# Kernel tuning notes

Measured on AMD Instinct MI355X. Metric: run time of the kernel, lower is better.

Reference implementation:

```python
import jax, jax.numpy as jnp
import numpy as np


def setup_inputs() -> dict:
    key = jax.random.key(0)
    k0, k1, k2, k3 = jax.random.split(key, 4)
    B, T, M, E, H = 4, 2048, 1024, 8, 4096
    x = jax.random.normal(k0, (B, T, M), dtype=jnp.float32)
    wg = jax.random.normal(k1, (M, E), dtype=jnp.float32) * 0.02
    w1 = jax.random.normal(k2, (E, M, H), dtype=jnp.float32) * 0.02
    w2 = jax.random.normal(k3, (E, H, M), dtype=jnp.float32) * 0.02
    return {"x": x, "wg": wg, "w1": w1, "w2": w2}


def reference(x, wg, w1, w2):
    """GShard MoE layer: top-1 gate + dense one-hot dispatch/combine + expert FFN."""
    M = x.shape[-1]
    xs = x.reshape(-1, M)                      # [s, m]
    s = xs.shape[0]
    E = wg.shape[1]
    capacity = s // E                          # capacity_factor = 1.0

    # ---- top-1 gate (deepspeed/gshard top1gating) ----
    logits = xs @ wg                           # [s, e]
    gates = jax.nn.softmax(logits, axis=-1)
    idx = jnp.argmax(gates, axis=1)            # [s]
    mask1 = jax.nn.one_hot(idx, E, dtype=gates.dtype)  # [s, e]
    me = gates.mean(axis=0)
    ce = mask1.mean(axis=0)
    l_aux = jnp.sum(me * ce) * E
    # position of each token within its expert's buffer
    locations = jnp.cumsum(mask1, axis=0) - 1.0          # [s, e]
    mask1 = mask1 * (locations < capacity).astype(gates.dtype)  # drop overflow
    gates1 = gates * mask1                                 # [s, e]
    loc_s = jnp.sum(locations * mask1, axis=1).astype(jnp.int32)  # [s]
    loc_sc = jax.nn.one_hot(loc_s, capacity, dtype=gates.dtype)   # [s, c]
    combine = gates1[:, :, None] * loc_sc[:, None, :]       # [s, e, c]
    dispatch = (combine > 0).astype(x.dtype)                # [s, e, c]

    # ---- dense one-hot dispatch (the kernel-headroom hotspot) ----
    dispatched = jnp.einsum('sec,sm->ecm', dispatch, xs)    # [e, c, m]

    # ---- per-expert 2-layer FFN ----
    h = jax.nn.relu(jnp.einsum('ecm,emh->ech', dispatched, w1))
    expert_out = jnp.einsum('ech,ehm->ecm', h, w2)          # [e, c, m]

    # ---- dense one-hot combine ----
    out = jnp.einsum('sec,ecm->sm', combine, expert_out).reshape(x.shape)
    return out, l_aux
```

## Files before the change

kernel.cpp:

```cpp
#include <hip/hip_runtime.h>
#include <hip/hip_bf16.h>

#define S_TOK 8192
#define MDIM  1024
#define EXP   8
#define HDIM  4096
#define CAP   1024

typedef __attribute__((ext_vector_type(8))) short short8;
typedef __attribute__((ext_vector_type(4))) float floatx4;

#define BARRIER() asm volatile("s_barrier" ::: "memory")
#define WAITV6()  asm volatile("s_waitcnt vmcnt(6)" ::: "memory")
#define WAITV0()  asm volatile("s_waitcnt vmcnt(0)" ::: "memory")
#define SCHEDB()  __builtin_amdgcn_sched_barrier(0)

__device__ __forceinline__ unsigned short f2b(float f) {
    union { float f; unsigned int i; } v; v.f = f;
    unsigned int r = v.i + 0x7fffu + ((v.i >> 16) & 1u);
    return (unsigned short)(r >> 16);
}

__device__ __forceinline__ void gl2lds16(const unsigned short* g, unsigned short* l) {
    __builtin_amdgcn_global_load_lds(
        (const __attribute__((address_space(1))) unsigned int*)g,
        (__attribute__((address_space(3))) unsigned int*)l,
        16, 0, 0);
}

__global__ __launch_bounds__(256) void gate_kernel(
    const float* __restrict__ x, const float* __restrict__ wg,
    float* __restrict__ gates8, int* __restrict__ token_expert)
{
    const int wave = threadIdx.x >> 6, lane = threadIdx.x & 63;
    const int s = blockIdx.x * 4 + wave;

    const float* xr = x + (size_t)s * MDIM + lane * 16;
    float xv[16];
#pragma unroll
    for (int q = 0; q < 4; ++q) *(float4*)(xv + q * 4) = *(const float4*)(xr + q * 4);

    float acc[EXP];
#pragma unroll
    for (int e = 0; e < EXP; ++e) acc[e] = 0.f;
    const int m0 = lane * 16;
#pragma unroll
    for (int j = 0; j < 16; ++j) {
        const float xm = xv[j];
        const float* wr = wg + (size_t)(m0 + j) * EXP;
        float4 w0 = *(const float4*)(wr);
        float4 w1v = *(const float4*)(wr + 4);
        acc[0] += xm * w0.x; acc[1] += xm * w0.y; acc[2] += xm * w0.z; acc[3] += xm * w0.w;
        acc[4] += xm * w1v.x; acc[5] += xm * w1v.y; acc[6] += xm * w1v.z; acc[7] += xm * w1v.w;
    }
#pragma unroll
    for (int e = 0; e < EXP; ++e) {
#pragma unroll
        for (int off = 32; off > 0; off >>= 1)
            acc[e] += __shfl_down(acc[e], off);
    }
    if (lane == 0) {
        float mx = acc[0]; int idx = 0;
#pragma unroll
        for (int e = 1; e < EXP; ++e) if (acc[e] > mx) { mx = acc[e]; idx = e; }
        float g[EXP]; float sum = 0.f;
#pragma unroll
        for (int e = 0; e < EXP; ++e) { g[e] = expf(acc[e] - mx); sum += g[e]; }
        float inv = 1.f / sum;
#pragma unroll
        for (int e = 0; e < EXP; ++e) gates8[(size_t)s * EXP + e] = g[e] * inv;
        token_expert[s] = idx;
    }
}

__global__ __launch_bounds__(256) void scan_kernel(
    const float* __restrict__ gates8, const int* __restrict__ token_expert,
    int* __restrict__ slot_token, float* __restrict__ slot_gate,
    float* __restrict__ laux_out)
{
    __shared__ int   cnt[256][EXP];
    __shared__ float fsum[256][EXP];
    __shared__ int   tot[EXP];
    const int t = threadIdx.x;

    for (int i = t; i < EXP * CAP; i += 256) slot_token[i] = -1;

    int local[EXP];
#pragma unroll
    for (int e = 0; e < EXP; ++e) local[e] = 0;
    const int s0 = t * 32;
    for (int j = 0; j < 32; ++j) local[token_expert[s0 + j]]++;
#pragma unroll
    for (int e = 0; e < EXP; ++e) cnt[t][e] = local[e];
    __syncthreads();

    if (t < EXP) {
        int run = 0;
        for (int i = 0; i < 256; ++i) { int v = cnt[i][t]; cnt[i][t] = run; run += v; }
        tot[t] = run;
    }
    __syncthreads();

    int off[EXP];
#pragma unroll
    for (int e = 0; e < EXP; ++e) off[e] = cnt[t][e];
    for (int j = 0; j < 32; ++j) {
        int s = s0 + j;
        int e = token_expert[s];
        int loc = off[e]++;
        if (loc < CAP) {
            int slot = e * CAP + loc;
            slot_token[slot] = s;
            slot_gate[slot]  = gates8[(size_t)s * EXP + e];
        }
    }

    float ms[EXP];
#pragma unroll
    for (int e = 0; e < EXP; ++e) ms[e] = 0.f;
    for (int j = 0; j < 32; ++j) {
        const float* g = gates8 + (size_t)(s0 + j) * EXP;
#pragma unroll
        for (int e = 0; e < EXP; ++e) ms[e] += g[e];
    }
#pragma unroll
    for (int e = 0; e < EXP; ++e) fsum[t][e] = ms[e];
    __syncthreads();
    for (int st = 128; st > 0; st >>= 1) {
        if (t < st) {
#pragma unroll
            for (int e = 0; e < EXP; ++e) fsum[t][e] += fsum[t + st][e];
        }
        __syncthreads();
    }
    if (t == 0) {
        float l = 0.f;
#pragma unroll
        for (int e = 0; e < EXP; ++e)
            l += (fsum[0][e] / (float)S_TOK) * ((float)tot[e] / (float)S_TOK);
        laux_out[0] = l * (float)EXP;
    }
}

__global__ __launch_bounds__(256) void dispatch_cvt(
    const float* __restrict__ x, const int* __restrict__ slot_token,
    unsigned short* __restrict__ xd)
{
    const int slot = blockIdx.x, t = threadIdx.x;
    const int tok = slot_token[slot];
    unsigned short v[4];
    if (tok >= 0) {
        float4 f = *(const float4*)(x + (size_t)tok * MDIM + t * 4);
        v[0] = f2b(f.x); v[1] = f2b(f.y); v[2] = f2b(f.z); v[3] = f2b(f.w);
    } else {
        v[0] = v[1] = v[2] = v[3] = 0;
    }
    *(int2*)(xd + (size_t)slot * MDIM + t * 4) = *(const int2*)v;
}

__global__ __launch_bounds__(256) void transpose_cvt(
    const float* __restrict__ src, unsigned short* __restrict__ dst, int R, int C)
{
    __shared__ unsigned short Ls[64 * 72];
    const size_t eo = (size_t)blockIdx.z * R * C;
    src += eo; dst += eo;
    const int C0 = blockIdx.x * 64, R0 = blockIdx.y * 64;
    const int t = threadIdx.x;
    {
        const int r = t >> 2, c0 = (t & 3) * 16;
        const float* p = src + (size_t)(R0 + r) * C + C0 + c0;
        float f[16];
#pragma unroll
        for (int q = 0; q < 4; ++q) *(float4*)(f + q * 4) = ((const float4*)p)[q];
#pragma unroll
        for (int j = 0; j < 16; ++j) Ls[(c0 + j) * 72 + r] = f2b(f[j]);
    }
    __syncthreads();
    {
        const int c = t >> 2, m0 = (t & 3) * 16;
        int4 v0 = *(const int4*)&Ls[c * 72 + m0];
        int4 v1 = *(const int4*)&Ls[c * 72 + m0 + 8];
        int4* q = (int4*)(dst + (size_t)(C0 + c) * R + R0 + m0);
        q[0] = v0; q[1] = v1;
    }
}

template<int KT, int N, bool SCATTER>
__global__ __launch_bounds__(512, 2) void ffn_gemm_8p(
    const unsigned short* __restrict__ Ag, const unsigned short* __restrict__ BT,
    void* __restrict__ Outv,
    const int* __restrict__ slot_token, const float* __restrict__ slot_gate)
{
    constexpr int K   = KT * 64;
    constexpr int NBX = N / 128;
    constexpr int NWG = NBX * (CAP / 256);

    extern __shared__ __align__(16) unsigned short sm[];
    unsigned short* Abuf = sm;
    unsigned short* Bbuf = sm + 3 * 16384;

    const int e    = blockIdx.z;
    const int orig = blockIdx.x;
    const int logical = (orig & 7) * (NWG >> 3) + (orig >> 3);
    const int nb = (logical % NBX) * 128;
    const int ib = (logical / NBX) * 256;

    const int tid  = threadIdx.x;
    const int lane = tid & 63, wave = tid >> 6;
    const int quad = lane >> 4, l15 = lane & 15;
    const int wm = wave >> 2, wn = wave & 3;

    const int rr   = tid >> 3;
    const int slot = (tid & 7) ^ (rr & 7);
    const unsigned short* Asrc = Ag + (size_t)(e * CAP + ib + rr) * K + slot * 8;
    const unsigned short* Bsrc = BT + ((size_t)e * N + nb + rr) * K + slot * 8;

    auto stageA = [&](int buf, int t, int ca) {
        gl2lds16(Asrc + (size_t)ca * 64 * K + t * 64,
                 Abuf + buf * 16384 + ca * 4096 + wave * 512);
    };
    auto stageB = [&](int buf, int t, int cb) {
        gl2lds16(Bsrc + (size_t)cb * 64 * K + t * 64,
                 Bbuf + buf * 8192 + cb * 4096 + wave * 512);
    };

    const int sx  = l15 & 7;
    const int ko0 = ((0 + quad) ^ sx) * 8;
    const int ko1 = ((4 + quad) ^ sx) * 8;
    const int arow = wm * 128 + l15;
    const int brow = wn * 32 + l15;

    floatx4 acc[8][2];
#pragma unroll
    for (int i = 0; i < 8; ++i)
#pragma unroll
        for (int j = 0; j < 2; ++j)
            acc[i][j] = (floatx4){0.f, 0.f, 0.f, 0.f};

#pragma unroll
    for (int ca = 0; ca < 4; ++ca) stageA(0, 0, ca);
#pragma unroll
    for (int cb = 0; cb < 2; ++cb) stageB(0, 0, cb);
#pragma unroll
    for (int ca = 0; ca < 4; ++ca) stageA(1, 1, ca);
#pragma unroll
    for (int cb = 0; cb < 2; ++cb) stageB(1, 1, cb);
    WAITV6();
    BARRIER();

    int buf = 0;
    for (int t = 0; t < KT; ++t) {
        const int nbuf = (buf >= 1) ? buf - 1 : 2;
        const bool st  = (t + 2 < KT);

        short8 brg[2][2];
#pragma unroll
        for (int fn = 0; fn < 2; ++fn) {
            const int row = brow + fn * 16;
            brg[fn][0] = *(const short8*)&Bbuf[buf * 8192 + row * 64 + ko0];
            brg[fn][1] = *(const short8*)&Bbuf[buf * 8192 + row * 64 + ko1];
        }
        short8 aA[8];
#pragma unroll
        for (int fm = 0; fm < 4; ++fm) {
            const int row = arow + fm * 16;
            aA[fm * 2 + 0] = *(const short8*)&Abuf[buf * 16384 + row * 64 + ko0];
            aA[fm * 2 + 1] = *(const short8*)&Abuf[buf * 16384 + row * 64 + ko1];
        }
        if (st) { stageA(nbuf, t + 2, 0); stageA(nbuf, t + 2, 1); }
        BARRIER(); SCHEDB();
        __builtin_amdgcn_s_setprio(1);
#pragma unroll
        for (int fm = 0; fm < 4; ++fm) {
            acc[fm][0] = __builtin_amdgcn_mfma_f32_16x16x32_bf16(aA[fm*2+0], brg[0][0], acc[fm][0], 0, 0, 0);
            acc[fm][0] = __builtin_amdgcn_mfma_f32_16x16x32_bf16(aA[fm*2+1], brg[0][1], acc[fm][0], 0, 0, 0);
        }
        __builtin_amdgcn_s_setprio(0); SCHEDB(); BARRIER();

        short8 aB[8];
#pragma unroll
        for (int fm = 0; fm < 4; ++fm) {
            const int row = arow + 64 + fm * 16;
            aB[fm * 2 + 0] = *(const short8*)&Abuf[buf * 16384 + row * 64 + ko0];
            aB[fm * 2 + 1] = *(const short8*)&Abuf[buf * 16384 + row * 64 + ko1];
        }
        if (st) { stageA(nbuf, t + 2, 2); stageA(nbuf, t + 2, 3); }
        BARRIER(); SCHEDB();
        __builtin_amdgcn_s_setprio(1);
#pragma unroll
        for (int fm = 0; fm < 4; ++fm) {
            acc[fm][1] = __builtin_amdgcn_mfma_f32_16x16x32_bf16(aA[fm*2+0], brg[1][0], acc[fm][1], 0, 0, 0);
            acc[fm][1] = __builtin_amdgcn_mfma_f32_16x16x32_bf16(aA[fm*2+1], brg[1][1], acc[fm][1], 0, 0, 0);
        }
        __builtin_amdgcn_s_setprio(0); SCHEDB(); BARRIER();

        if (st) stageB(nbuf, t + 2, 0);
        BARRIER(); SCHEDB();
        __builtin_amdgcn_s_setprio(1);
#pragma unroll
        for (int fm = 0; fm < 4; ++fm) {
            acc[4+fm][0] = __builtin_amdgcn_mfma_f32_16x16x32_bf16(aB[fm*2+0], brg[0][0], acc[4+fm][0], 0, 0, 0);
            acc[4+fm][0] = __builtin_amdgcn_mfma_f32_16x16x32_bf16(aB[fm*2+1], brg[0][1], acc[4+fm][0], 0, 0, 0);
        }
        __builtin_amdgcn_s_setprio(0); SCHEDB(); BARRIER();

        if (st) stageB(nbuf, t + 2, 1);
        BARRIER(); SCHEDB();
        __builtin_amdgcn_s_setprio(1);
#pragma unroll
        for (int fm = 0; fm < 4; ++fm) {
            acc[4+fm][1] = __builtin_amdgcn_mfma_f32_16x16x32_bf16(aB[fm*2+0], brg[1][0], acc[4+fm][1], 0, 0, 0);
            acc[4+fm][1] = __builtin_amdgcn_mfma_f32_16x16x32_bf16(aB[fm*2+1], brg[1][1], acc[4+fm][1], 0, 0, 0);
        }
        __builtin_amdgcn_s_setprio(0); SCHEDB();
        if (t + 1 < KT) {
            if (st) WAITV6(); else WAITV0();
            BARRIER();
        }
        buf = (buf == 2) ? 0 : buf + 1;
    }

#pragma unroll
    for (int FM = 0; FM < 8; ++FM) {
        const int rowb = ib + wm * 128 + FM * 16 + quad * 4;
#pragma unroll
        for (int r = 0; r < 4; ++r) {
            const int gi = rowb + r;
            if (SCATTER) {
                const int slotI = e * CAP + gi;
                const int tok = slot_token[slotI];
                if (tok >= 0) {
                    const float gsc = slot_gate[slotI];
                    float* Out = (float*)Outv;
#pragma unroll
                    for (int fn = 0; fn < 2; ++fn) {
                        const int gn = nb + wn * 32 + fn * 16 + l15;
                        Out[(size_t)tok * N + gn] = gsc * acc[FM][fn][r];
                    }
                }
            } else {
                unsigned short* Out = (unsigned short*)Outv;
#pragma unroll
                for (int fn = 0; fn < 2; ++fn) {
                    const int gn = nb + wn * 32 + fn * 16 + l15;
                    Out[((size_t)e * CAP + gi) * N + gn] = f2b(fmaxf(acc[FM][fn][r], 0.f));
                }
            }
        }
    }
}

template<int KSTEPS, int N, bool SCATTER>
__global__ __launch_bounds__(256) void ffn_gemm_fast(
    const unsigned short* __restrict__ Ab, const unsigned short* __restrict__ BT,
    void* __restrict__ Outv,
    const int* __restrict__ slot_token, const float* __restrict__ slot_gate)
{
    constexpr int K = KSTEPS * 32;
    const int e  = blockIdx.z;
    const int ib = blockIdx.y * 128;
    const int nb = blockIdx.x * 128;
    const int t  = threadIdx.x;

    __shared__ unsigned short As[2][128 * 32];
    __shared__ unsigned short Bs[2][128 * 32];

    const int lane = t & 63, wave = t >> 6;
    const int quad = lane >> 4, l15 = lane & 15;
    const int wr = wave >> 1, wc = wave & 1;

    const int c0    = wave * 2;
    const int srow  = lane >> 2;
    const int kpart = (lane & 3) * 8;

    const unsigned short* Ag = Ab + (size_t)(e * CAP + ib) * K + kpart;
    const unsigned short* Bg = BT + ((size_t)e * N + nb) * K + kpart;
    const size_t row0 = (size_t)(c0 * 16 + srow) * K;
    const size_t row1 = (size_t)(c0 * 16 + 16 + srow) * K;

    floatx4 acc[4][4];
#pragma unroll
    for (int r = 0; r < 4; ++r)
#pragma unroll
        for (int c = 0; c < 4; ++c)
            acc[r][c] = (floatx4){0.f, 0.f, 0.f, 0.f};

    auto stage = [&](int buf, int kb) {
        const int k0 = kb * 32;
        gl2lds16(Ag + row0 + k0, &As[buf][(c0    ) * 512]);
        gl2lds16(Ag + row1 + k0, &As[buf][(c0 + 1) * 512]);
        gl2lds16(Bg + row0 + k0, &Bs[buf][(c0    ) * 512]);
        gl2lds16(Bg + row1 + k0, &Bs[buf][(c0 + 1) * 512]);
    };

    int cur = 0;
    stage(0, 0);
    __syncthreads();

    for (int kb = 0; kb < KSTEPS; ++kb) {
        if (kb + 1 < KSTEPS) stage(cur ^ 1, kb + 1);

        short8 af[4], bfr[4];
#pragma unroll
        for (int r = 0; r < 4; ++r)
            af[r] = *(const short8*)&As[cur][(wr * 64 + r * 16 + l15) * 32 + quad * 8];
#pragma unroll
        for (int c = 0; c < 4; ++c)
            bfr[c] = *(const short8*)&Bs[cur][(wc * 64 + c * 16 + l15) * 32 + quad * 8];
#pragma unroll
        for (int r = 0; r < 4; ++r)
#pragma unroll
            for (int c = 0; c < 4; ++c)
                acc[r][c] = __builtin_amdgcn_mfma_f32_16x16x32_bf16(af[r], bfr[c], acc[r][c], 0, 0, 0);

        __syncthreads();
        cur ^= 1;
    }

#pragma unroll
    for (int r = 0; r < 4; ++r) {
#pragma unroll
        for (int reg = 0; reg < 4; ++reg) {
            const int gi = ib + wr * 64 + r * 16 + quad * 4 + reg;
            if (SCATTER) {
                const int slot = e * CAP + gi;
                const int tok = slot_token[slot];
                if (tok >= 0) {
                    const float gsc = slot_gate[slot];
                    float* Out = (float*)Outv;
#pragma unroll
                    for (int c = 0; c < 4; ++c) {
                        const int gn = nb + wc * 64 + c * 16 + l15;
                        Out[(size_t)tok * N + gn] = gsc * acc[r][c][reg];
                    }
                }
            } else {
                unsigned short* Out = (unsigned short*)Outv;
#pragma unroll
                for (int c = 0; c < 4; ++c) {
                    const int gn = nb + wc * 64 + c * 16 + l15;
                    Out[((size_t)e * CAP + gi) * N + gn] = f2b(fmaxf(acc[r][c][reg], 0.f));
                }
            }
        }
    }
}

template<int KSTEPS, int N, bool GATHER, bool SCATTER>
__global__ __launch_bounds__(256) void ffn_gemm_slow(
    const void* __restrict__ Agv, const float* __restrict__ Bg,
    void* __restrict__ Outv,
    const int* __restrict__ slot_token, const float* __restrict__ slot_gate)
{
    constexpr int K = KSTEPS * 32;
    const int e  = blockIdx.z;
    const int ib = blockIdx.y * 128;
    const int nb = blockIdx.x * 128;
    const int t  = threadIdx.x;

    __shared__ unsigned short As[128 * 40];
    __shared__ unsigned short Bs[32 * 136];

    const float* B = Bg + (size_t)e * K * N;
    const int arow  = t >> 1;
    const int ahalf = t & 1;
    const float* ArowF = nullptr;
    const unsigned short* ArowH = nullptr;
    bool avalid = true;
    if (GATHER) {
        int tok = slot_token[e * CAP + ib + arow];
        avalid = (tok >= 0);
        ArowF = (const float*)Agv + (size_t)(avalid ? tok : 0) * K;
    } else {
        ArowH = (const unsigned short*)Agv + ((size_t)e * CAP + ib + arow) * K;
    }
    const int bk  = t >> 3;
    const int bn0 = (t & 7) * 16;
    const float* Bptr = B + (size_t)bk * N + nb + bn0;

    const int lane = t & 63, wave = t >> 6;
    const int quad = lane >> 4, l15 = lane & 15;
    const int wr = wave >> 1, wc = wave & 1;

    floatx4 acc[4][4];
#pragma unroll
    for (int r = 0; r < 4; ++r)
#pragma unroll
        for (int c = 0; c < 4; ++c)
            acc[r][c] = (floatx4){0.f, 0.f, 0.f, 0.f};

    for (int kb = 0; kb < KSTEPS; ++kb) {
        const int k0 = kb * 32;
        unsigned short av[16];
        if (GATHER) {
            if (avalid) {
                const float4* p = (const float4*)(ArowF + k0 + ahalf * 16);
                float4 f0 = p[0], f1 = p[1], f2 = p[2], f3 = p[3];
                const float fa[16] = {f0.x,f0.y,f0.z,f0.w, f1.x,f1.y,f1.z,f1.w,
                                      f2.x,f2.y,f2.z,f2.w, f3.x,f3.y,f3.z,f3.w};
#pragma unroll
                for (int j = 0; j < 16; ++j) av[j] = f2b(fa[j]);
            } else {
#pragma unroll
                for (int j = 0; j < 16; ++j) av[j] = 0;
            }
        } else {
            const int4* p = (const int4*)(ArowH + k0 + ahalf * 16);
            *(int4*)(av)     = p[0];
            *(int4*)(av + 8) = p[1];
        }
        unsigned short bv[16];
        {
            const float4* q = (const float4*)(Bptr + (size_t)k0 * N);
            float4 f0 = q[0], f1 = q[1], f2 = q[2], f3 = q[3];
            const float fb[16] = {f0.x,f0.y,f0.z,f0.w, f1.x,f1.y,f1.z,f1.w,
                                  f2.x,f2.y,f2.z,f2.w, f3.x,f3.y,f3.z,f3.w};
#pragma unroll
            for (int j = 0; j < 16; ++j) bv[j] = f2b(fb[j]);
        }

        *(int4*)&As[arow * 40 + ahalf * 16]     = *(int4*)(av);
        *(int4*)&As[arow * 40 + ahalf * 16 + 8] = *(int4*)(av + 8);
        *(int4*)&Bs[bk * 136 + bn0]             = *(int4*)(bv);
        *(int4*)&Bs[bk * 136 + bn0 + 8]         = *(int4*)(bv + 8);
        __syncthreads();

        short8 af[4];
#pragma unroll
        for (int r = 0; r < 4; ++r)
            af[r] = *(const short8*)&As[(wr * 64 + r * 16 + l15) * 40 + quad * 8];
        short8 bfr[4];
#pragma unroll
        for (int c = 0; c < 4; ++c) {
#pragma unroll
            for (int j = 0; j < 8; ++j)
                bfr[c][j] = (short)Bs[(quad * 8 + j) * 136 + wc * 64 + c * 16 + l15];
        }
#pragma unroll
        for (int r = 0; r < 4; ++r)
#pragma unroll
            for (int c = 0; c < 4; ++c)
                acc[r][c] = __builtin_amdgcn_mfma_f32_16x16x32_bf16(af[r], bfr[c], acc[r][c], 0, 0, 0);
        __syncthreads();
    }

#pragma unroll
    for (int r = 0; r < 4; ++r) {
#pragma unroll
        for (int reg = 0; reg < 4; ++reg) {
            const int gi = ib + wr * 64 + r * 16 + quad * 4 + reg;
            if (SCATTER) {
                const int slot = e * CAP + gi;
                const int tok = slot_token[slot];
                if (tok >= 0) {
                    const float gsc = slot_gate[slot];
                    float* Out = (float*)Outv;
#pragma unroll
                    for (int c = 0; c < 4; ++c) {
                        const int gn = nb + wc * 64 + c * 16 + l15;
                        Out[(size_t)tok * N + gn] = gsc * acc[r][c][reg];
                    }
                }
            } else {
                unsigned short* Out = (unsigned short*)Outv;
#pragma unroll
                for (int c = 0; c < 4; ++c) {
                    const int gn = nb + wc * 64 + c * 16 + l15;
                    Out[((size_t)e * CAP + gi) * N + gn] = f2b(fmaxf(acc[r][c][reg], 0.f));
                }
            }
        }
    }
}

extern "C" void kernel_launch(void* const* d_in, const int* in_sizes, int n_in,
                              void* d_out, int out_size, void* d_ws, size_t ws_size,
                              hipStream_t stream)
{
    const float* x  = (const float*)d_in[0];
    const float* wg = (const float*)d_in[1];
    const float* w1 = (const float*)d_in[2];
    const float* w2 = (const float*)d_in[3];
    float* out = (float*)d_out;

    char* ws = (char*)d_ws;
    float* gates8       = (float*)(ws);
    int*   token_expert = (int*)(ws + 262144);
    int*   slot_token   = (int*)(ws + 294912);
    float* slot_gate    = (float*)(ws + 327680);

    hipMemsetAsync(d_out, 0, (size_t)out_size * 4, stream);
    gate_kernel<<<dim3(S_TOK / 4), dim3(256), 0, stream>>>(x, wg, gates8, token_expert);
    scan_kernel<<<dim3(1), dim3(256), 0, stream>>>(gates8, token_expert, slot_token, slot_gate,
                                                   out + (size_t)S_TOK * MDIM);

    const size_t FAST_NEED = 151355392ull;
    if (ws_size >= FAST_NEED) {
        unsigned short* xd = (unsigned short*)(ws + 360448);
        unsigned short* h  = (unsigned short*)(ws + 17137664);
        unsigned short* W  = (unsigned short*)(ws + 84246528);

        static bool tried = false, ok8 = false;
        if (!tried) {
            tried = true;
            ok8 = (hipFuncSetAttribute((const void*)ffn_gemm_8p<16, HDIM, false>,
                       hipFuncAttributeMaxDynamicSharedMemorySize, 147456) == hipSuccess)
               && (hipFuncSetAttribute((const void*)ffn_gemm_8p<64, MDIM, true>,
                       hipFuncAttributeMaxDynamicSharedMemorySize, 147456) == hipSuccess);
        }

        dispatch_cvt<<<dim3(EXP * CAP), dim3(256), 0, stream>>>(x, slot_token, xd);
        transpose_cvt<<<dim3(HDIM / 64, MDIM / 64, EXP), dim3(256), 0, stream>>>(w1, W, MDIM, HDIM);
        if (ok8) {
            ffn_gemm_8p<16, HDIM, false><<<dim3((HDIM/128) * (CAP/256), 1, EXP), dim3(512), 147456, stream>>>(
                xd, W, h, slot_token, slot_gate);
        } else {
            ffn_gemm_fast<32, HDIM, false><<<dim3(HDIM / 128, CAP / 128, EXP), dim3(256), 0, stream>>>(
                xd, W, h, slot_token, slot_gate);
        }
        transpose_cvt<<<dim3(MDIM / 64, HDIM / 64, EXP), dim3(256), 0, stream>>>(w2, W, HDIM, MDIM);
        if (ok8) {
            ffn_gemm_8p<64, MDIM, true><<<dim3((MDIM/128) * (CAP/256), 1, EXP), dim3(512), 147456, stream>>>(
                h, W, out, slot_token, slot_gate);
        } else {
            ffn_gemm_fast<128, MDIM, true><<<dim3(MDIM / 128, CAP / 128, EXP), dim3(256), 0, stream>>>(
                h, W, out, slot_token, slot_gate);
        }
    } else {
        unsigned short* h = (unsigned short*)(ws + 360448);
        ffn_gemm_slow<32, HDIM, true, false><<<dim3(HDIM / 128, CAP / 128, EXP), dim3(256), 0, stream>>>(
            x, w1, h, slot_token, slot_gate);
        ffn_gemm_slow<128, MDIM, false, true><<<dim3(MDIM / 128, CAP / 128, EXP), dim3(256), 0, stream>>>(
            h, w2, out, slot_token, slot_gate);
    }
}
```

Before: 568.9 us.

## Fuse scan, output zeroing and weight transposes into one prep launch; gather in GEMM

The gate kernel now also writes a bf16 copy of x. A single mega_prep launch does four jobs: block 0 runs the routing scan, other blocks zero the output, and the rest transpose and convert w1, plus w2 when the workspace is large enough. This replaces the separate memset, scan, dispatch and transpose launches. The first FFN GEMM gathers token rows directly through slot_token instead of reading a separately dispatched buffer. The aim is to cut launch count and stop the one-block scan from serializing the pipeline, at the cost of computing junk rows for empty slots and depending on workspace size for the wide path.

```diff
diff --git a/kernel.cpp b/kernel.cpp
--- a/kernel.cpp
+++ b/kernel.cpp
@@ -30,7 +30,8 @@
 
 __global__ __launch_bounds__(256) void gate_kernel(
     const float* __restrict__ x, const float* __restrict__ wg,
-    float* __restrict__ gates8, int* __restrict__ token_expert)
+    float* __restrict__ gates8, int* __restrict__ token_expert,
+    unsigned short* __restrict__ xb16)
 {
     const int wave = threadIdx.x >> 6, lane = threadIdx.x & 63;
     const int s = blockIdx.x * 4 + wave;
@@ -39,6 +40,15 @@
     float xv[16];
 #pragma unroll
     for (int q = 0; q < 4; ++q) *(float4*)(xv + q * 4) = *(const float4*)(xr + q * 4);
+
+    if (xb16) {
+        unsigned short bv[16];
+#pragma unroll
+        for (int j = 0; j < 16; ++j) bv[j] = f2b(xv[j]);
+        int4* dst = (int4*)(xb16 + (size_t)s * MDIM + lane * 16);
+        dst[0] = ((const int4*)bv)[0];
+        dst[1] = ((const int4*)bv)[1];
+    }
 
     float acc[EXP];
 #pragma unroll
@@ -70,6 +80,326 @@
 #pragma unroll
         for (int e = 0; e < EXP; ++e) gates8[(size_t)s * EXP + e] = g[e] * inv;
         token_expert[s] = idx;
+    }
+}
+
+__device__ __forceinline__ void transpose_tile(
+    const float* __restrict__ src, unsigned short* __restrict__ dst,
+    int R, int C, int R0, int C0, unsigned short* Ls)
+{
+    const int t = threadIdx.x;
+    {
+        const int r = t >> 2, c0 = (t & 3) * 16;
+        const float* p = src + (size_t)(R0 + r) * C + C0 + c0;
+        float f[16];
+#pragma unroll
+        for (int q = 0; q < 4; ++q) *(float4*)(f + q * 4) = ((const float4*)p)[q];
+#pragma unroll
+        for (int j = 0; j < 16; ++j) Ls[(c0 + j) * 72 + r] = f2b(f[j]);
+    }
+    __syncthreads();
+    {
+        const int c = t >> 2, m0 = (t & 3) * 16;
+        int4 v0 = *(const int4*)&Ls[c * 72 + m0];
+        int4 v1 = *(const int4*)&Ls[c * 72 + m0 + 8];
+        int4* q = (int4*)(dst + (size_t)(C0 + c) * R + R0 + m0);
+        q[0] = v0; q[1] = v1;
+    }
+}
+
+__global__ __launch_bounds__(256) void mega_prep(
+    const float* __restrict__ gates8, const int* __restrict__ token_expert,
+    int* __restrict__ slot_token, float* __restrict__ slot_gate,
+    float* __restrict__ laux_out,
+    const float* __restrict__ w1, const float* __restrict__ w2,
+    unsigned short* __restrict__ W1T, unsigned short* __restrict__ W2T,
+    float* __restrict__ outz)
+{
+    __shared__ int            cntS[256 * EXP];
+    __shared__ float          fsumS[256 * EXP];
+    __shared__ unsigned short Ls[64 * 72];
+
+    const int b = blockIdx.x;
+    const int t = threadIdx.x;
+
+    if (b == 0) {
+        for (int i = t; i < EXP * CAP; i += 256) slot_token[i] = -1;
+
+        int local[EXP];
+#pragma unroll
+        for (int e = 0; e < EXP; ++e) local[e] = 0;
+        const int s0 = t * 32;
+        for (int j = 0; j < 32; ++j) local[token_expert[s0 + j]]++;
+
+        int incl[EXP];
+#pragma unroll
+        for (int e = 0; e < EXP; ++e) { incl[e] = local[e]; cntS[t * EXP + e] = incl[e]; }
+        __syncthreads();
+        for (int d = 1; d < 256; d <<= 1) {
+            int add[EXP];
+            if (t >= d) {
+#pragma unroll
+                for (int e = 0; e < EXP; ++e) add[e] = cntS[(t - d) * EXP + e];
+            }
+            __syncthreads();
+            if (t >= d) {
+#pragma unroll
+                for (int e = 0; e < EXP; ++e) { incl[e] += add[e]; cntS[t * EXP + e] = incl[e]; }
+            }
+            __syncthreads();
+        }
+
+        int off[EXP];
+#pragma unroll
+        for (int e = 0; e < EXP; ++e) off[e] = incl[e] - local[e];
+        for (int j = 0; j < 32; ++j) {
+            int s = s0 + j;
+            int e = token_expert[s];
+            int loc = off[e]++;
+            if (loc < CAP) {
+                int slot = e * CAP + loc;
+                slot_token[slot] = s;
+                slot_gate[slot]  = gates8[(size_t)s * EXP + e];
+            }
+        }
+
+        float ms[EXP];
+#pragma unroll
+        for (int e = 0; e < EXP; ++e) ms[e] = 0.f;
+        for (int j = 0; j < 32; ++j) {
+            const float* g = gates8 + (size_t)(s0 + j) * EXP;
+#pragma unroll
+            for (int e = 0; e < EXP; ++e) ms[e] += g[e];
+        }
+#pragma unroll
+        for (int e = 0; e < EXP; ++e) fsumS[t * EXP + e] = ms[e];
+        __syncthreads();
+        for (int st = 128; st > 0; st >>= 1) {
+            if (t < st) {
+#pragma unroll
+                for (int e = 0; e < EXP; ++e) fsumS[t * EXP + e] += fsumS[(t + st) * EXP + e];
+            }
+            __syncthreads();
+        }
+        if (t == 0) {
+            float l = 0.f;
+#pragma unroll
+            for (int e = 0; e < EXP; ++e)
+                l += (fsumS[e] / (float)S_TOK) * ((float)cntS[255 * EXP + e] / (float)S_TOK);
+            laux_out[0] = l * (float)EXP;
+        }
+        return;
+    }
+
+    if (b <= 2048) {
+        float4* p = (float4*)(outz + (size_t)(b - 1) * 4096 + t * 16);
+        const float4 z = {0.f, 0.f, 0.f, 0.f};
+        p[0] = z; p[1] = z; p[2] = z; p[3] = z;
+        return;
+    }
+
+    int i = b - 2049;
+    if (i < 8192) {
+        const int e = i >> 10, rem = i & 1023;
+        const int bx = rem & 63, by = rem >> 6;
+        transpose_tile(w1 + (size_t)e * MDIM * HDIM, W1T + (size_t)e * MDIM * HDIM,
+                       MDIM, HDIM, by * 64, bx * 64, Ls);
+        return;
+    }
+    i -= 8192;
+    {
+        const int e = i >> 10, rem = i & 1023;
+        const int bx = rem & 15, by = rem >> 4;
+        transpose_tile(w2 + (size_t)e * MDIM * HDIM, W2T + (size_t)e * MDIM * HDIM,
+                       HDIM, MDIM, by * 64, bx * 64, Ls);
+    }
+}
+
+__global__ __launch_bounds__(256) void transpose_cvt(
+    const float* __restrict__ src, unsigned short* __restrict__ dst, int R, int C)
+{
+    __shared__ unsigned short Ls[64 * 72];
+    const size_t eo = (size_t)blockIdx.z * R * C;
+    transpose_tile(src + eo, dst + eo, R, C, blockIdx.y * 64, blockIdx.x * 64, Ls);
+}
+
+template<int KT, int N, bool SCATTER, bool GATHER>
+__global__ __launch_bounds__(512, 2) void ffn_gemm_8p(
+    const unsigned short* __restrict__ Ag, const unsigned short* __restrict__ BT,
+    void* __restrict__ Outv,
+    const int* __restrict__ slot_token, const float* __restrict__ slot_gate)
+{
+    constexpr int K   = KT * 64;
+    constexpr int NBX = N / 128;
+    constexpr int NWG = NBX * (CAP / 256);
+
+    extern __shared__ __align__(16) unsigned short sm[];
+    unsigned short* Abuf = sm;
+    unsigned short* Bbuf = sm + 3 * 16384;
+
+    const int e    = blockIdx.z;
+    const int orig = blockIdx.x;
+    const int logical = (orig & 7) * (NWG >> 3) + (orig >> 3);
+    const int nb = (logical % NBX) * 128;
+    const int ib = (logical / NBX) * 256;
+
+    const int tid  = threadIdx.x;
+    const int lane = tid & 63, wave = tid >> 6;
+    const int quad = lane >> 4, l15 = lane & 15;
+    const int wm = wave >> 2, wn = wave & 3;
+
+    const int rr   = tid >> 3;
+    const int slot = (tid & 7) ^ (rr & 7);
+
+    const unsigned short* sA0;
+    const unsigned short* sA1;
+    const unsigned short* sA2;
+    const unsigned short* sA3;
+    if (GATHER) {
+        const int base = e * CAP + ib + rr;
+        int t0 = slot_token[base];
+        int t1 = slot_token[base + 64];
+        int t2 = slot_token[base + 128];
+        int t3 = slot_token[base + 192];
+        sA0 = Ag + (size_t)(t0 < 0 ? 0 : t0) * K + slot * 8;
+        sA1 = Ag + (size_t)(t1 < 0 ? 0 : t1) * K + slot * 8;
+        sA2 = Ag + (size_t)(t2 < 0 ? 0 : t2) * K + slot * 8;
+        sA3 = Ag + (size_t)(t3 < 0 ? 0 : t3) * K + slot * 8;
+    } else {
+        sA0 = Ag + (size_t)(e * CAP + ib + rr) * K + slot * 8;
+        sA1 = sA0 + (size_t)64 * K;
+        sA2 = sA0 + (size_t)128 * K;
+        sA3 = sA0 + (size_t)192 * K;
+    }
+    const unsigned short* Bsrc = BT + ((size_t)e * N + nb + rr) * K + slot * 8;
+
+    auto stageA = [&](int buf, int t, const unsigned short* s, int ca) {
+        gl2lds16(s + t * 64, Abuf + buf * 16384 + ca * 4096 + wave * 512);
+    };
+    auto stageB = [&](int buf, int t, int cb) {
+        gl2lds16(Bsrc + (size_t)cb * 64 * K + t * 64,
+                 Bbuf + buf * 8192 + cb * 4096 + wave * 512);
+    };
+
+    const int sx  = l15 & 7;
+    const int ko0 = ((0 + quad) ^ sx) * 8;
+    const int ko1 = ((4 + quad) ^ sx) * 8;
+    const int arow = wm * 128 + l15;
+    const int brow = wn * 32 + l15;
+
+    floatx4 acc[8][2];
+#pragma unroll
+    for (int i = 0; i < 8; ++i)
+#pragma unroll
+        for (int j = 0; j < 2; ++j)
+            acc[i][j] = (floatx4){0.f, 0.f, 0.f, 0.f};
+
+    stageA(0, 0, sA0, 0); stageA(0, 0, sA1, 1); stageA(0, 0, sA2, 2); stageA(0, 0, sA3, 3);
+    stageB(0, 0, 0); stageB(0, 0, 1);
+    stageA(1, 1, sA0, 0); stageA(1, 1, sA1, 1); stageA(1, 1, sA2, 2); stageA(1, 1, sA3, 3);
+    stageB(1, 1, 0); stageB(1, 1, 1);
+    WAITV6();
+    BARRIER();
+
+    int buf = 0;
+    for (int t = 0; t < KT; ++t) {
+        const int nbuf = (buf >= 1) ? buf - 1 : 2;
+        const bool st  = (t + 2 < KT);
+
+        short8 brg[2][2];
+#pragma unroll
+        for (int fn = 0; fn < 2; ++fn) {
+            const int row = brow + fn * 16;
+            brg[fn][0] = *(const short8*)&Bbuf[buf * 8192 + row * 64 + ko0];
+            brg[fn][1] = *(const short8*)&Bbuf[buf * 8192 + row * 64 + ko1];
+        }
+        short8 aA[8];
+#pragma unroll
+        for (int fm = 0; fm < 4; ++fm) {
+            const int row = arow + fm * 16;
+            aA[fm * 2 + 0] = *(const short8*)&Abuf[buf * 16384 + row * 64 + ko0];
+            aA[fm * 2 + 1] = *(const short8*)&Abuf[buf * 16384 + row * 64 + ko1];
+        }
+        if (st) { stageA(nbuf, t + 2, sA0, 0); stageA(nbuf, t + 2, sA1, 1); }
+        BARRIER(); SCHEDB();
+        __builtin_amdgcn_s_setprio(1);
+#pragma unroll
+        for (int fm = 0; fm < 4; ++fm) {
+            acc[fm][0] = __builtin_amdgcn_mfma_f32_16x16x32_bf16(aA[fm*2+0], brg[0][0], acc[fm][0], 0, 0, 0);
+            acc[fm][0] = __builtin_amdgcn_mfma_f32_16x16x32_bf16(aA[fm*2+1], brg[0][1], acc[fm][0], 0, 0, 0);
+        }
+        __builtin_amdgcn_s_setprio(0); SCHEDB(); BARRIER();
+
+        short8 aB[8];
+#pragma unroll
+        for (int fm = 0; fm < 4; ++fm) {
+            const int row = arow + 64 + fm * 16;
+            aB[fm * 2 + 0] = *(const short8*)&Abuf[buf * 16384 + row * 64 + ko0];
+            aB[fm * 2 + 1] = *(const short8*)&Abuf[buf * 16384 + row * 64 + ko1];
+        }
+        if (st) { stageA(nbuf, t + 2, sA2, 2); stageA(nbuf, t + 2, sA3, 3); }
+        BARRIER(); SCHEDB();
+        __builtin_amdgcn_s_setprio(1);
+#pragma unroll
+        for (int fm = 0; fm < 4; ++fm) {
+            acc[fm][1] = __builtin_amdgcn_mfma_f32_16x16x32_bf16(aA[fm*2+0], brg[1][0], acc[fm][1], 0, 0, 0);
+            acc[fm][1] = __builtin_amdgcn_mfma_f32_16x16x32_bf16(aA[fm*2+1], brg[1][1], acc[fm][1], 0, 0, 0);
+        }
+        __builtin_amdgcn_s_setprio(0); SCHEDB(); BARRIER();
+
+        if (st) stageB(nbuf, t + 2, 0);
+        BARRIER(); SCHEDB();
+        __builtin_amdgcn_s_setprio(1);
+#pragma unroll
+        for (int fm = 0; fm < 4; ++fm) {
+            acc[4+fm][0] = __builtin_amdgcn_mfma_f32_16x16x32_bf16(aB[fm*2+0], brg[0][0], acc[4+fm][0], 0, 0, 0);
+            acc[4+fm][0] = __builtin_amdgcn_mfma_f32_16x16x32_bf16(aB[fm*2+1], brg[0][1], acc[4+fm][0], 0, 0, 0);
+        }
+        __builtin_amdgcn_s_setprio(0); SCHEDB(); BARRIER();
+
+        if (st) stageB(nbuf, t + 2, 1);
+        BARRIER(); SCHEDB();
+        __builtin_amdgcn_s_setprio(1);
+#pragma unroll
+        for (int fm = 0; fm < 4; ++fm) {
+            acc[4+fm][1] = __builtin_amdgcn_mfma_f32_16x16x32_bf16(aB[fm*2+0], brg[1][0], acc[4+fm][1], 0, 0, 0);
+            acc[4+fm][1] = __builtin_amdgcn_mfma_f32_16x16x32_bf16(aB[fm*2+1], brg[1][1], acc[4+fm][1], 0, 0, 0);
+        }
+        __builtin_amdgcn_s_setprio(0); SCHEDB();
+        if (t + 1 < KT) {
+            if (st) WAITV6(); else WAITV0();
+            BARRIER();
+        }
+        buf = (buf == 2) ? 0 : buf + 1;
+    }
+
+#pragma unroll
+    for (int FM = 0; FM < 8; ++FM) {
+        const int rowb = ib + wm * 128 + FM * 16 + quad * 4;
+#pragma unroll
+        for (int r = 0; r < 4; ++r) {
+            const int gi = rowb + r;
+            if (SCATTER) {
+                const int slotI = e * CAP + gi;
+                const int tok = slot_token[slotI];
+                if (tok >= 0) {
+                    const float gsc = slot_gate[slotI];
+                    float* Out = (float*)Outv;
+#pragma unroll
+                    for (int fn = 0; fn < 2; ++fn) {
+                        const int gn = nb + wn * 32 + fn * 16 + l15;
+                        Out[(size_t)tok * N + gn] = gsc * acc[FM][fn][r];
+                    }
+                }
+            } else {
+                unsigned short* Out = (unsigned short*)Outv;
+#pragma unroll
+                for (int fn = 0; fn < 2; ++fn) {
+                    const int gn = nb + wn * 32 + fn * 16 + l15;
+                    Out[((size_t)e * CAP + gi) * N + gn] = f2b(fmaxf(acc[FM][fn][r], 0.f));
+                }
+            }
+        }
     }
 }
 
@@ -139,310 +469,6 @@
         for (int e = 0; e < EXP; ++e)
             l += (fsum[0][e] / (float)S_TOK) * ((float)tot[e] / (float)S_TOK);
         laux_out[0] = l * (float)EXP;
-    }
-}
-
-__global__ __launch_bounds__(256) void dispatch_cvt(
-    const float* __restrict__ x, const int* __restrict__ slot_token,
-    unsigned short* __restrict__ xd)
-{
-    const int slot = blockIdx.x, t = threadIdx.x;
-    const int tok = slot_token[slot];
-    unsigned short v[4];
-    if (tok >= 0) {
-        float4 f = *(const float4*)(x + (size_t)tok * MDIM + t * 4);
-        v[0] = f2b(f.x); v[1] = f2b(f.y); v[2] = f2b(f.z); v[3] = f2b(f.w);
-    } else {
-        v[0] = v[1] = v[2] = v[3] = 0;
-    }
-    *(int2*)(xd + (size_t)slot * MDIM + t * 4) = *(const int2*)v;
-}
-
-__global__ __launch_bounds__(256) void transpose_cvt(
-    const float* __restrict__ src, unsigned short* __restrict__ dst, int R, int C)
-{
-    __shared__ unsigned short Ls[64 * 72];
-    const size_t eo = (size_t)blockIdx.z * R * C;
-    src += eo; dst += eo;
-    const int C0 = blockIdx.x * 64, R0 = blockIdx.y * 64;
-    const int t = threadIdx.x;
-    {
-        const int r = t >> 2, c0 = (t & 3) * 16;
-        const float* p = src + (size_t)(R0 + r) * C + C0 + c0;
-        float f[16];
-#pragma unroll
-        for (int q = 0; q < 4; ++q) *(float4*)(f + q * 4) = ((const float4*)p)[q];
-#pragma unroll
-        for (int j = 0; j < 16; ++j) Ls[(c0 + j) * 72 + r] = f2b(f[j]);
-    }
-    __syncthreads();
-    {
-        const int c = t >> 2, m0 = (t & 3) * 16;
-        int4 v0 = *(const int4*)&Ls[c * 72 + m0];
-        int4 v1 = *(const int4*)&Ls[c * 72 + m0 + 8];
-        int4* q = (int4*)(dst + (size_t)(C0 + c) * R + R0 + m0);
-        q[0] = v0; q[1] = v1;
-    }
-}
-
-template<int KT, int N, bool SCATTER>
-__global__ __launch_bounds__(512, 2) void ffn_gemm_8p(
-    const unsigned short* __restrict__ Ag, const unsigned short* __restrict__ BT,
-    void* __restrict__ Outv,
-    const int* __restrict__ slot_token, const float* __restrict__ slot_gate)
-{
-    constexpr int K   = KT * 64;
-    constexpr int NBX = N / 128;
-    constexpr int NWG = NBX * (CAP / 256);
-
-    extern __shared__ __align__(16) unsigned short sm[];
-    unsigned short* Abuf = sm;
-    unsigned short* Bbuf = sm + 3 * 16384;
-
-    const int e    = blockIdx.z;
-    const int orig = blockIdx.x;
-    const int logical = (orig & 7) * (NWG >> 3) + (orig >> 3);
-    const int nb = (logical % NBX) * 128;
-    const int ib = (logical / NBX) * 256;
-
-    const int tid  = threadIdx.x;
-    const int lane = tid & 63, wave = tid >> 6;
-    const int quad = lane >> 4, l15 = lane & 15;
-    const int wm = wave >> 2, wn = wave & 3;
-
-    const int rr   = tid >> 3;
-    const int slot = (tid & 7) ^ (rr & 7);
-    const unsigned short* Asrc = Ag + (size_t)(e * CAP + ib + rr) * K + slot * 8;
-    const unsigned short* Bsrc = BT + ((size_t)e * N + nb + rr) * K + slot * 8;
-
-    auto stageA = [&](int buf, int t, int ca) {
-        gl2lds16(Asrc + (size_t)ca * 64 * K + t * 64,
-                 Abuf + buf * 16384 + ca * 4096 + wave * 512);
-    };
-    auto stageB = [&](int buf, int t, int cb) {
-        gl2lds16(Bsrc + (size_t)cb * 64 * K + t * 64,
-                 Bbuf + buf * 8192 + cb * 4096 + wave * 512);
-    };
-
-    const int sx  = l15 & 7;
-    const int ko0 = ((0 + quad) ^ sx) * 8;
-    const int ko1 = ((4 + quad) ^ sx) * 8;
-    const int arow = wm * 128 + l15;
-    const int brow = wn * 32 + l15;
-
-    floatx4 acc[8][2];
-#pragma unroll
-    for (int i = 0; i < 8; ++i)
-#pragma unroll
-        for (int j = 0; j < 2; ++j)
-            acc[i][j] = (floatx4){0.f, 0.f, 0.f, 0.f};
-
-#pragma unroll
-    for (int ca = 0; ca < 4; ++ca) stageA(0, 0, ca);
-#pragma unroll
-    for (int cb = 0; cb < 2; ++cb) stageB(0, 0, cb);
-#pragma unroll
-    for (int ca = 0; ca < 4; ++ca) stageA(1, 1, ca);
-#pragma unroll
-    for (int cb = 0; cb < 2; ++cb) stageB(1, 1, cb);
-    WAITV6();
-    BARRIER();
-
-    int buf = 0;
-    for (int t = 0; t < KT; ++t) {
-        const int nbuf = (buf >= 1) ? buf - 1 : 2;
-        const bool st  = (t + 2 < KT);
-
-        short8 brg[2][2];
-#pragma unroll
-        for (int fn = 0; fn < 2; ++fn) {
-            const int row = brow + fn * 16;
-            brg[fn][0] = *(const short8*)&Bbuf[buf * 8192 + row * 64 + ko0];
-            brg[fn][1] = *(const short8*)&Bbuf[buf * 8192 + row * 64 + ko1];
-        }
-        short8 aA[8];
-#pragma unroll
-        for (int fm = 0; fm < 4; ++fm) {
-            const int row = arow + fm * 16;
-            aA[fm * 2 + 0] = *(const short8*)&Abuf[buf * 16384 + row * 64 + ko0];
-            aA[fm * 2 + 1] = *(const short8*)&Abuf[buf * 16384 + row * 64 + ko1];
-        }
-        if (st) { stageA(nbuf, t + 2, 0); stageA(nbuf, t + 2, 1); }
-        BARRIER(); SCHEDB();
-        __builtin_amdgcn_s_setprio(1);
-#pragma unroll
-        for (int fm = 0; fm < 4; ++fm) {
-            acc[fm][0] = __builtin_amdgcn_mfma_f32_16x16x32_bf16(aA[fm*2+0], brg[0][0], acc[fm][0], 0, 0, 0);
-            acc[fm][0] = __builtin_amdgcn_mfma_f32_16x16x32_bf16(aA[fm*2+1], brg[0][1], acc[fm][0], 0, 0, 0);
-        }
-        __builtin_amdgcn_s_setprio(0); SCHEDB(); BARRIER();
-
-        short8 aB[8];
-#pragma unroll
-        for (int fm = 0; fm < 4; ++fm) {
-            const int row = arow + 64 + fm * 16;
-            aB[fm * 2 + 0] = *(const short8*)&Abuf[buf * 16384 + row * 64 + ko0];
-            aB[fm * 2 + 1] = *(const short8*)&Abuf[buf * 16384 + row * 64 + ko1];
-        }
-        if (st) { stageA(nbuf, t + 2, 2); stageA(nbuf, t + 2, 3); }
-        BARRIER(); SCHEDB();
-        __builtin_amdgcn_s_setprio(1);
-#pragma unroll
-        for (int fm = 0; fm < 4; ++fm) {
-            acc[fm][1] = __builtin_amdgcn_mfma_f32_16x16x32_bf16(aA[fm*2+0], brg[1][0], acc[fm][1], 0, 0, 0);
-            acc[fm][1] = __builtin_amdgcn_mfma_f32_16x16x32_bf16(aA[fm*2+1], brg[1][1], acc[fm][1], 0, 0, 0);
-        }
-        __builtin_amdgcn_s_setprio(0); SCHEDB(); BARRIER();
-
-        if (st) stageB(nbuf, t + 2, 0);
-        BARRIER(); SCHEDB();
-        __builtin_amdgcn_s_setprio(1);
-#pragma unroll
-        for (int fm = 0; fm < 4; ++fm) {
-            acc[4+fm][0] = __builtin_amdgcn_mfma_f32_16x16x32_bf16(aB[fm*2+0], brg[0][0], acc[4+fm][0], 0, 0, 0);
-            acc[4+fm][0] = __builtin_amdgcn_mfma_f32_16x16x32_bf16(aB[fm*2+1], brg[0][1], acc[4+fm][0], 0, 0, 0);
-        }
-        __builtin_amdgcn_s_setprio(0); SCHEDB(); BARRIER();
-
-        if (st) stageB(nbuf, t + 2, 1);
-        BARRIER(); SCHEDB();
-        __builtin_amdgcn_s_setprio(1);
-#pragma unroll
-        for (int fm = 0; fm < 4; ++fm) {
-            acc[4+fm][1] = __builtin_amdgcn_mfma_f32_16x16x32_bf16(aB[fm*2+0], brg[1][0], acc[4+fm][1], 0, 0, 0);
-            acc[4+fm][1] = __builtin_amdgcn_mfma_f32_16x16x32_bf16(aB[fm*2+1], brg[1][1], acc[4+fm][1], 0, 0, 0);
-        }
-        __builtin_amdgcn_s_setprio(0); SCHEDB();
-        if (t + 1 < KT) {
-            if (st) WAITV6(); else WAITV0();
-            BARRIER();
-        }
-        buf = (buf == 2) ? 0 : buf + 1;
-    }
-
-#pragma unroll
-    for (int FM = 0; FM < 8; ++FM) {
-        const int rowb = ib + wm * 128 + FM * 16 + quad * 4;
-#pragma unroll
-        for (int r = 0; r < 4; ++r) {
-            const int gi = rowb + r;
-            if (SCATTER) {
-                const int slotI = e * CAP + gi;
-                const int tok = slot_token[slotI];
-                if (tok >= 0) {
-                    const float gsc = slot_gate[slotI];
-                    float* Out = (float*)Outv;
-#pragma unroll
-                    for (int fn = 0; fn < 2; ++fn) {
-                        const int gn = nb + wn * 32 + fn * 16 + l15;
-                        Out[(size_t)tok * N + gn] = gsc * acc[FM][fn][r];
-                    }
-                }
-            } else {
-                unsigned short* Out = (unsigned short*)Outv;
-#pragma unroll
-                for (int fn = 0; fn < 2; ++fn) {
-                    const int gn = nb + wn * 32 + fn * 16 + l15;
-                    Out[((size_t)e * CAP + gi) * N + gn] = f2b(fmaxf(acc[FM][fn][r], 0.f));
-                }
-            }
-        }
-    }
-}
-
-template<int KSTEPS, int N, bool SCATTER>
-__global__ __launch_bounds__(256) void ffn_gemm_fast(
-    const unsigned short* __restrict__ Ab, const unsigned short* __restrict__ BT,
-    void* __restrict__ Outv,
-    const int* __restrict__ slot_token, const float* __restrict__ slot_gate)
-{
-    constexpr int K = KSTEPS * 32;
-    const int e  = blockIdx.z;
-    const int ib = blockIdx.y * 128;
-    const int nb = blockIdx.x * 128;
-    const int t  = threadIdx.x;
-
-    __shared__ unsigned short As[2][128 * 32];
-    __shared__ unsigned short Bs[2][128 * 32];
-
-    const int lane = t & 63, wave = t >> 6;
-    const int quad = lane >> 4, l15 = lane & 15;
-    const int wr = wave >> 1, wc = wave & 1;
-
-    const int c0    = wave * 2;
-    const int srow  = lane >> 2;
-    const int kpart = (lane & 3) * 8;
-
-    const unsigned short* Ag = Ab + (size_t)(e * CAP + ib) * K + kpart;
-    const unsigned short* Bg = BT + ((size_t)e * N + nb) * K + kpart;
-    const size_t row0 = (size_t)(c0 * 16 + srow) * K;
-    const size_t row1 = (size_t)(c0 * 16 + 16 + srow) * K;
-
-    floatx4 acc[4][4];
-#pragma unroll
-    for (int r = 0; r < 4; ++r)
-#pragma unroll
-        for (int c = 0; c < 4; ++c)
-            acc[r][c] = (floatx4){0.f, 0.f, 0.f, 0.f};
-
-    auto stage = [&](int buf, int kb) {
-        const int k0 = kb * 32;
-        gl2lds16(Ag + row0 + k0, &As[buf][(c0    ) * 512]);
-        gl2lds16(Ag + row1 + k0, &As[buf][(c0 + 1) * 512]);
-        gl2lds16(Bg + row0 + k0, &Bs[buf][(c0    ) * 512]);
-        gl2lds16(Bg + row1 + k0, &Bs[buf][(c0 + 1) * 512]);
-    };
-
-    int cur = 0;
-    stage(0, 0);
-    __syncthreads();
-
-    for (int kb = 0; kb < KSTEPS; ++kb) {
-        if (kb + 1 < KSTEPS) stage(cur ^ 1, kb + 1);
-
-        short8 af[4], bfr[4];
-#pragma unroll
-        for (int r = 0; r < 4; ++r)
-            af[r] = *(const short8*)&As[cur][(wr * 64 + r * 16 + l15) * 32 + quad * 8];
-#pragma unroll
-        for (int c = 0; c < 4; ++c)
-            bfr[c] = *(const short8*)&Bs[cur][(wc * 64 + c * 16 + l15) * 32 + quad * 8];
-#pragma unroll
-        for (int r = 0; r < 4; ++r)
-#pragma unroll
-            for (int c = 0; c < 4; ++c)
-                acc[r][c] = __builtin_amdgcn_mfma_f32_16x16x32_bf16(af[r], bfr[c], acc[r][c], 0, 0, 0);
-
-        __syncthreads();
-        cur ^= 1;
-    }
-
-#pragma unroll
-    for (int r = 0; r < 4; ++r) {
-#pragma unroll
-        for (int reg = 0; reg < 4; ++reg) {
-            const int gi = ib + wr * 64 + r * 16 + quad * 4 + reg;
-            if (SCATTER) {
-                const int slot = e * CAP + gi;
-                const int tok = slot_token[slot];
-                if (tok >= 0) {
-                    const float gsc = slot_gate[slot];
-                    float* Out = (float*)Outv;
-#pragma unroll
-                    for (int c = 0; c < 4; ++c) {
-                        const int gn = nb + wc * 64 + c * 16 + l15;
-                        Out[(size_t)tok * N + gn] = gsc * acc[r][c][reg];
-                    }
-                }
-            } else {
-                unsigned short* Out = (unsigned short*)Outv;
-#pragma unroll
-                for (int c = 0; c < 4; ++c) {
-                    const int gn = nb + wc * 64 + c * 16 + l15;
-                    Out[((size_t)e * CAP + gi) * N + gn] = f2b(fmaxf(acc[r][c][reg], 0.f));
-                }
-            }
-        }
     }
 }
 
@@ -582,55 +608,61 @@
     const float* w1 = (const float*)d_in[2];
     const float* w2 = (const float*)d_in[3];
     float* out = (float*)d_out;
+    float* laux = out + (size_t)S_TOK * MDIM;
 
     char* ws = (char*)d_ws;
     float* gates8       = (float*)(ws);
     int*   token_expert = (int*)(ws + 262144);
     int*   slot_token   = (int*)(ws + 294912);
     float* slot_gate    = (float*)(ws + 327680);
-
-    hipMemsetAsync(d_out, 0, (size_t)out_size * 4, stream);
-    gate_kernel<<<dim3(S_TOK / 4), dim3(256), 0, stream>>>(x, wg, gates8, token_expert);
-    scan_kernel<<<dim3(1), dim3(256), 0, stream>>>(gates8, token_expert, slot_token, slot_gate,
-                                                   out + (size_t)S_TOK * MDIM);
+    unsigned short* xb16 = (unsigned short*)(ws + 360448);
+    unsigned short* h    = (unsigned short*)(ws + 17137664);
+    unsigned short* W1T  = (unsigned short*)(ws + 84246528);
+    unsigned short* W2T  = (unsigned short*)(ws + 151355392);
 
     const size_t FAST_NEED = 151355392ull;
+    const size_t WIDE_NEED = 218464256ull;
+
     if (ws_size >= FAST_NEED) {
-        unsigned short* xd = (unsigned short*)(ws + 360448);
-        unsigned short* h  = (unsigned short*)(ws + 17137664);
-        unsigned short* W  = (unsigned short*)(ws + 84246528);
+        const bool wide = (ws_size >= WIDE_NEED);
 
         static bool tried = false, ok8 = false;
         if (!tried) {
             tried = true;
-            ok8 = (hipFuncSetAttribute((const void*)ffn_gemm_8p<16, HDIM, false>,
+            ok8 = (hipFuncSetAttribute((const void*)ffn_gemm_8p<16, HDIM, false, true>,
                        hipFuncAttributeMaxDynamicSharedMemorySize, 147456) == hipSuccess)
-               && (hipFuncSetAttribute((const void*)ffn_gemm_8p<64, MDIM, true>,
+               && (hipFuncSetAttribute((const void*)ffn_gemm_8p<64, MDIM, true, false>,
                        hipFuncAttributeMaxDynamicSharedMemorySize, 147456) == hipSuccess);
         }
 
-        dispatch_cvt<<<dim3(EXP * CAP), dim3(256), 0, stream>>>(x, slot_token, xd);
-        transpose_cvt<<<dim3(HDIM / 64, MDIM / 64, EXP), dim3(256), 0, stream>>>(w1, W, MDIM, HDIM);
+        gate_kernel<<<dim3(S_TOK / 4), dim3(256), 0, stream>>>(x, wg, gates8, token_expert, xb16);
+
+        const int nblk = 1 + 2048 + 8192 + (wide ? 8192 : 0);
+        mega_prep<<<dim3(nblk), dim3(256), 0, stream>>>(
+            gates8, token_expert, slot_token, slot_gate, laux,
+            w1, w2, W1T, wide ? W2T : W1T, out);
+
         if (ok8) {
-            ffn_gemm_8p<16, HDIM, false><<<dim3((HDIM/128) * (CAP/256), 1, EXP), dim3(512), 147456, stream>>>(
-                xd, W, h, slot_token, slot_gate);
+            ffn_gemm_8p<16, HDIM, false, true><<<dim3((HDIM/128)*(CAP/256), 1, EXP), dim3(512), 147456, stream>>>(
+                xb16, W1T, h, slot_token, slot_gate);
+            if (!wide)
+                transpose_cvt<<<dim3(MDIM / 64, HDIM / 64, EXP), dim3(256), 0, stream>>>(w2, W1T, HDIM, MDIM);
+            ffn_gemm_8p<64, MDIM, true, false><<<dim3((MDIM/128)*(CAP/256), 1, EXP), dim3(512), 147456, stream>>>(
+                h, wide ? W2T : W1T, out, slot_token, slot_gate);
         } else {
-            ffn_gemm_fast<32, HDIM, false><<<dim3(HDIM / 128, CAP / 128, EXP), dim3(256), 0, stream>>>(
-                xd, W, h, slot_token, slot_gate);
-        }
-        transpose_cvt<<<dim3(MDIM / 64, HDIM / 64, EXP), dim3(256), 0, stream>>>(w2, W, HDIM, MDIM);
-        if (ok8) {
-            ffn_gemm_8p<64, MDIM, true><<<dim3((MDIM/128) * (CAP/256), 1, EXP), dim3(512), 147456, stream>>>(
-                h, W, out, slot_token, slot_gate);
-        } else {
-            ffn_gemm_fast<128, MDIM, true><<<dim3(MDIM / 128, CAP / 128, EXP), dim3(256), 0, stream>>>(
-                h, W, out, slot_token, slot_gate);
+            ffn_gemm_slow<32, HDIM, true, false><<<dim3(HDIM / 128, CAP / 128, EXP), dim3(256), 0, stream>>>(
+                x, w1, h, slot_token, slot_gate);
+            ffn_gemm_slow<128, MDIM, false, true><<<dim3(MDIM / 128, CAP / 128, EXP), dim3(256), 0, stream>>>(
+                h, w2, out, slot_token, slot_gate);
         }
     } else {
-        unsigned short* h = (unsigned short*)(ws + 360448);
+        hipMemsetAsync(d_out, 0, (size_t)out_size * 4, stream);
+        gate_kernel<<<dim3(S_TOK / 4), dim3(256), 0, stream>>>(x, wg, gates8, token_expert, nullptr);
+        scan_kernel<<<dim3(1), dim3(256), 0, stream>>>(gates8, token_expert, slot_token, slot_gate, laux);
+        unsigned short* hs = (unsigned short*)(ws + 360448);
         ffn_gemm_slow<32, HDIM, true, false><<<dim3(HDIM / 128, CAP / 128, EXP), dim3(256), 0, stream>>>(
-            x, w1, h, slot_token, slot_gate);
+            x, w1, hs, slot_token, slot_gate);
         ffn_gemm_slow<128, MDIM, false, true><<<dim3(MDIM / 128, CAP / 128, EXP), dim3(256), 0, stream>>>(
-            h, w2, out, slot_token, slot_gate);
-    }
-}
+            hs, w2, out, slot_token, slot_gate);
+    }
+}
```

Result: faster. 549.4 us (-3.4%).
